# Kernel tuning notes

Hardware: AMD Instinct MI355X
Metric: run time of the kernel (lower is better)

The kernel has to match this reference:

```python
import jax, jax.numpy as jnp
import numpy as np

T, BATCH, DIM = 2048, 32, 512

def setup_inputs() -> dict:
    key = jax.random.key(0)
    ks = jax.random.split(key, 9)
    s = 1.0 / np.sqrt(DIM)
    return {
        "x": jax.random.normal(ks[0], (T, BATCH, DIM), dtype=jnp.float32),
        "W_in": jax.random.uniform(ks[1], (2 * DIM, DIM), jnp.float32, -s, s),
        "b_in": jax.random.uniform(ks[2], (2 * DIM,), jnp.float32, -s, s),
        "W_out": jax.random.uniform(ks[3], (DIM, DIM), jnp.float32, -s, s),
        "b_out": jax.random.uniform(ks[4], (DIM,), jnp.float32, -s, s),
        "A": jax.random.normal(ks[5], (DIM,), dtype=jnp.float32) * 0.1,
        "B": jax.random.normal(ks[6], (DIM,), dtype=jnp.float32) * 0.1,
        "gamma": jnp.ones((DIM,), dtype=jnp.float32),
        "beta": jnp.zeros((DIM,), dtype=jnp.float32),
    }

def _layernorm(y, gamma, beta, eps=1e-5):
    mu = jnp.mean(y, axis=-1, keepdims=True)
    var = jnp.mean(jnp.square(y - mu), axis=-1, keepdims=True)
    return (y - mu) * jax.lax.rsqrt(var + eps) * gamma + beta

def reference(x, W_in, b_in, W_out, b_out, A, B, gamma, beta):
    # in_proj then chunk along last dim: z first half, g second half
    zg = jnp.einsum('tbd,ed->tbe', x, W_in) + b_in          # [T,B,2D]
    z, g = jnp.split(zg, 2, axis=-1)
    g = jax.nn.sigmoid(g)
    Bz = B * z                                              # [T,B,D]
    gA = g * A                                              # [T,B,D]

    # diagonal linear recurrence h_t = gA_t * h_{t-1} + Bz_t
    def step(prev, inp):
        ga_t, bz_t = inp
        curr = ga_t * prev + bz_t
        return curr, curr

    h0 = jnp.zeros((x.shape[1], x.shape[2]), dtype=x.dtype)
    _, h = jax.lax.scan(step, h0, (gA, Bz))                 # [T,B,D]

    out = jnp.einsum('tbd,ed->tbe', h, W_out) + b_out
    return _layernorm(x + out, gamma, beta)
```

## Files before the change

kernel.cpp:

```cpp
#include <hip/hip_runtime.h>
#include <hip/hip_bf16.h>
#include <cstdint>
#include <cstddef>

#define T_LEN 2048
#define BATCH 32
#define DIM 512
#define M_TOT (T_LEN * BATCH)
#define K_DIM DIM
#define N1 (2 * DIM)
#define NCHUNK 64
#define CLEN (T_LEN / NCHUNK)
#define BD (BATCH * DIM)
#define MT256 (M_TOT / 256)

typedef unsigned short ushort_t;
typedef __attribute__((ext_vector_type(8))) short short8;
typedef __attribute__((ext_vector_type(4))) float floatx4;
typedef __attribute__((ext_vector_type(4))) unsigned short ushort4v;

__device__ __forceinline__ float bf2f(ushort_t u) {
  union { unsigned int i; float f; } v;
  v.i = ((unsigned int)u) << 16;
  return v.f;
}
__device__ __forceinline__ ushort_t f2bf(float f) {
  union { float f; unsigned int i; } v;
  v.f = f;
  unsigned int x = v.i;
  return (ushort_t)((x + 0x7fffu + ((x >> 16) & 1u)) >> 16);
}

__device__ __forceinline__ void async16(const void* gp, void* lp) {
  __builtin_amdgcn_global_load_lds(
      (__attribute__((address_space(1))) void*)(void*)gp,
      (__attribute__((address_space(3))) void*)lp, 16, 0, 0);
}

#define WAITVM(N) asm volatile("s_waitcnt vmcnt(" #N ")" ::: "memory")

__global__ __launch_bounds__(256) void cvt_f32_bf16(const float* __restrict__ in,
                                                    ushort_t* __restrict__ out,
                                                    int n4) {
  int i = blockIdx.x * 256 + threadIdx.x;
  if (i >= n4) return;
  const floatx4 v = *((const floatx4*)in + i);
  ushort4v o;
  o.x = f2bf(v.x); o.y = f2bf(v.y); o.z = f2bf(v.z); o.w = f2bf(v.w);
  *((ushort4v*)out + i) = o;
}

template <int MODE, int NT>
__global__ __launch_bounds__(512, 2) void gemm_bt(
    const ushort_t* __restrict__ Ag, const ushort_t* __restrict__ Bg,
    const float* __restrict__ bias, const float* __restrict__ Avec,
    const float* __restrict__ Bvec, ushort_t* __restrict__ out0,
    ushort_t* __restrict__ out1) {
  __shared__ __align__(16) ushort_t As[2][256 * 64];
  __shared__ __align__(16) ushort_t Bs[2][256 * 64];
  const int tid = threadIdx.x;
  const int lane = tid & 63;
  const int wid = tid >> 6;
  const int wave_m = wid >> 2;
  const int wave_n = wid & 3;

  const int bid = blockIdx.x;
  const int xcd = bid & 7;
  const int slot = bid >> 3;
  const int mt = xcd * (MT256 / 8) + slot / NT;
  const int nt = slot % NT;
  const int m0 = mt * 256;
  const int n0 = nt * 256;

  floatx4 acc[8][4] = {};

  const int sr = tid >> 3;
  const int sc = tid & 7;

  auto stage = [&](int kt, int s) {
    const int k0 = kt * 64;
#pragma unroll
    for (int i = 0; i < 4; i++) {
      const int r = i * 64 + sr;
      const int cg = sc ^ (r & 7);
      async16(Ag + (size_t)(m0 + r) * K_DIM + k0 + cg * 8,
              (char*)(&As[s][0]) + (i * 64 + wid * 8) * 128);
      async16(Bg + (size_t)(n0 + r) * K_DIM + k0 + cg * 8,
              (char*)(&Bs[s][0]) + (i * 64 + wid * 8) * 128);
    }
  };

  stage(0, 0);

  for (int t = 0; t < K_DIM / 64; ++t) {
    if (t < K_DIM / 64 - 1) {
      stage(t + 1, (t + 1) & 1);
      WAITVM(8);
    } else {
      WAITVM(0);
    }
    __builtin_amdgcn_s_barrier();
    __builtin_amdgcn_sched_barrier(0);

    const ushort_t* Asl = &As[t & 1][0];
    const ushort_t* Bsl = &Bs[t & 1][0];
#pragma unroll
    for (int kk = 0; kk < 2; kk++) {
      const int jc = kk * 4 + (lane >> 4);
      short8 af[8], bfr[4];
#pragma unroll
      for (int im = 0; im < 8; im++) {
        const int row = wave_m * 128 + im * 16 + (lane & 15);
        af[im] = *(const short8*)((const char*)Asl + row * 128 +
                                  ((jc ^ (row & 7)) * 16));
      }
#pragma unroll
      for (int in = 0; in < 4; in++) {
        const int row = wave_n * 64 + in * 16 + (lane & 15);
        bfr[in] = *(const short8*)((const char*)Bsl + row * 128 +
                                   ((jc ^ (row & 7)) * 16));
      }
#pragma unroll
      for (int im = 0; im < 8; im++)
#pragma unroll
        for (int in = 0; in < 4; in++)
          acc[im][in] = __builtin_amdgcn_mfma_f32_16x16x32_bf16(
              af[im], bfr[in], acc[im][in], 0, 0, 0);
    }
    __builtin_amdgcn_sched_barrier(0);
    __builtin_amdgcn_s_barrier();
  }

#pragma unroll
  for (int im = 0; im < 8; im++) {
#pragma unroll
    for (int in = 0; in < 4; in++) {
      const int col = n0 + wave_n * 64 + in * 16 + (lane & 15);
#pragma unroll
      for (int r = 0; r < 4; r++) {
        const int row = m0 + wave_m * 128 + im * 16 + (lane >> 4) * 4 + r;
        float val = acc[im][in][r] + bias[col];
        if (MODE == 0) {
          if (col < DIM) {
            out0[(size_t)row * DIM + col] = f2bf(Bvec[col] * val);
          } else {
            const int d = col - DIM;
            const float s = 1.f / (1.f + __expf(-val));
            out1[(size_t)row * DIM + d] = f2bf(Avec[d] * s);
          }
        } else {
          out0[(size_t)row * DIM + col] = f2bf(val);
        }
      }
    }
  }
}


__global__ __launch_bounds__(256) void scan_pass1(
    const ushort_t* __restrict__ a_arr, const ushort_t* __restrict__ bz_arr,
    float* __restrict__ pout, float* __restrict__ hout) {
  const int tid = blockIdx.x * 256 + threadIdx.x;
  const int c = tid >> 12;
  const int q = tid & 4095;
  size_t base = (size_t)(c * CLEN) * BD + q * 4;
  float h0 = 0.f, h1 = 0.f, h2 = 0.f, h3 = 0.f;
  float p0 = 1.f, p1 = 1.f, p2 = 1.f, p3 = 1.f;
#pragma unroll 8
  for (int t = 0; t < CLEN; t++) {
    ushort4v av = *(const ushort4v*)(a_arr + base + (size_t)t * BD);
    ushort4v bv = *(const ushort4v*)(bz_arr + base + (size_t)t * BD);
    float a0 = bf2f(av.x), a1 = bf2f(av.y), a2 = bf2f(av.z), a3 = bf2f(av.w);
    h0 = a0 * h0 + bf2f(bv.x); p0 *= a0;
    h1 = a1 * h1 + bf2f(bv.y); p1 *= a1;
    h2 = a2 * h2 + bf2f(bv.z); p2 *= a2;
    h3 = a3 * h3 + bf2f(bv.w); p3 *= a3;
  }
  const size_t ci = (size_t)c * BD + q * 4;
  *(floatx4*)(pout + ci) = (floatx4){p0, p1, p2, p3};
  *(floatx4*)(hout + ci) = (floatx4){h0, h1, h2, h3};
}

__global__ __launch_bounds__(256) void scan_pass2(
    const float* __restrict__ p, const float* __restrict__ hend,
    float* __restrict__ carry) {
  const int q = blockIdx.x * 256 + threadIdx.x;
  float h0 = 0.f, h1 = 0.f, h2 = 0.f, h3 = 0.f;
  for (int c = 0; c < NCHUNK; c++) {
    const size_t ci = (size_t)c * BD + q * 4;
    floatx4 pv = *(const floatx4*)(p + ci);
    floatx4 hv = *(const floatx4*)(hend + ci);
    *(floatx4*)(carry + ci) = (floatx4){h0, h1, h2, h3};
    h0 = hv.x + pv.x * h0;
    h1 = hv.y + pv.y * h1;
    h2 = hv.z + pv.z * h2;
    h3 = hv.w + pv.w * h3;
  }
}

__global__ __launch_bounds__(256) void scan_pass3(
    const ushort_t* __restrict__ a_arr, const ushort_t* __restrict__ bz_arr,
    const float* __restrict__ carry, ushort_t* __restrict__ h_arr) {
  const int tid = blockIdx.x * 256 + threadIdx.x;
  const int c = tid >> 12;
  const int q = tid & 4095;
  size_t base = (size_t)(c * CLEN) * BD + q * 4;
  const size_t ci = (size_t)c * BD + q * 4;
  floatx4 cv = *(const floatx4*)(carry + ci);
  float h0 = cv.x, h1 = cv.y, h2 = cv.z, h3 = cv.w;
#pragma unroll 8
  for (int t = 0; t < CLEN; t++) {
    ushort4v av = *(const ushort4v*)(a_arr + base + (size_t)t * BD);
    ushort4v bv = *(const ushort4v*)(bz_arr + base + (size_t)t * BD);
    h0 = bf2f(av.x) * h0 + bf2f(bv.x);
    h1 = bf2f(av.y) * h1 + bf2f(bv.y);
    h2 = bf2f(av.z) * h2 + bf2f(bv.z);
    h3 = bf2f(av.w) * h3 + bf2f(bv.w);
    ushort4v o;
    o.x = f2bf(h0); o.y = f2bf(h1); o.z = f2bf(h2); o.w = f2bf(h3);
    *(ushort4v*)(h_arr + base + (size_t)t * BD) = o;
  }
}

__global__ __launch_bounds__(256) void ln_kernel(
    const float* __restrict__ x, const ushort_t* __restrict__ op,
    const float* __restrict__ gamma, const float* __restrict__ beta,
    float* __restrict__ y) {
  const int wid = threadIdx.x >> 6;
  const int lane = threadIdx.x & 63;
  const size_t row = (size_t)blockIdx.x * 4 + wid;
  const size_t base = row * DIM + lane * 8;
  floatx4 x0 = *(const floatx4*)(x + base);
  floatx4 x1 = *(const floatx4*)(x + base + 4);
  short8 ov = *(const short8*)(op + base);
  float v[8];
  v[0] = x0.x + bf2f((ushort_t)ov[0]);
  v[1] = x0.y + bf2f((ushort_t)ov[1]);
  v[2] = x0.z + bf2f((ushort_t)ov[2]);
  v[3] = x0.w + bf2f((ushort_t)ov[3]);
  v[4] = x1.x + bf2f((ushort_t)ov[4]);
  v[5] = x1.y + bf2f((ushort_t)ov[5]);
  v[6] = x1.z + bf2f((ushort_t)ov[6]);
  v[7] = x1.w + bf2f((ushort_t)ov[7]);
  float s = 0.f, ss = 0.f;
#pragma unroll
  for (int j = 0; j < 8; j++) {
    s += v[j];
    ss += v[j] * v[j];
  }
#pragma unroll
  for (int m = 32; m >= 1; m >>= 1) {
    s += __shfl_xor(s, m, 64);
    ss += __shfl_xor(ss, m, 64);
  }
  const float mean = s * (1.f / DIM);
  const float var = ss * (1.f / DIM) - mean * mean;
  const float rstd = rsqrtf(var + 1e-5f);
  const int cb = lane * 8;
  floatx4 o0, o1;
  o0.x = (v[0] - mean) * rstd * gamma[cb + 0] + beta[cb + 0];
  o0.y = (v[1] - mean) * rstd * gamma[cb + 1] + beta[cb + 1];
  o0.z = (v[2] - mean) * rstd * gamma[cb + 2] + beta[cb + 2];
  o0.w = (v[3] - mean) * rstd * gamma[cb + 3] + beta[cb + 3];
  o1.x = (v[4] - mean) * rstd * gamma[cb + 4] + beta[cb + 4];
  o1.y = (v[5] - mean) * rstd * gamma[cb + 5] + beta[cb + 5];
  o1.z = (v[6] - mean) * rstd * gamma[cb + 6] + beta[cb + 6];
  o1.w = (v[7] - mean) * rstd * gamma[cb + 7] + beta[cb + 7];
  *(floatx4*)(y + base) = o0;
  *(floatx4*)(y + base + 4) = o1;
}

extern "C" void kernel_launch(void* const* d_in, const int* in_sizes, int n_in,
                              void* d_out, int out_size, void* d_ws,
                              size_t ws_size, hipStream_t stream) {
  const float* x = (const float*)d_in[0];
  const float* W_in = (const float*)d_in[1];
  const float* b_in = (const float*)d_in[2];
  const float* W_out = (const float*)d_in[3];
  const float* b_out = (const float*)d_in[4];
  const float* Avec = (const float*)d_in[5];
  const float* Bvec = (const float*)d_in[6];
  const float* gamma = (const float*)d_in[7];
  const float* beta = (const float*)d_in[8];
  float* out = (float*)d_out;

  char* ws = (char*)d_ws;
  const size_t SZ64 = (size_t)M_TOT * DIM * 2;
  ushort_t* xb = (ushort_t*)ws;
  ushort_t* gA = (ushort_t*)(ws + SZ64);
  ushort_t* bz = (ushort_t*)(ws + 2 * SZ64);
  ushort_t* wib = (ushort_t*)(ws + 3 * SZ64);
  ushort_t* wob = (ushort_t*)(ws + 3 * SZ64 + (size_t)N1 * K_DIM * 2);
  char* p0 = ws + 3 * SZ64 + (size_t)N1 * K_DIM * 2 + (size_t)DIM * K_DIM * 2;
  float* pc = (float*)p0;
  float* hc = (float*)(p0 + (size_t)NCHUNK * BD * 4);
  float* cc = (float*)(p0 + 2 * (size_t)NCHUNK * BD * 4);

  cvt_f32_bf16<<<(M_TOT * DIM / 4 + 255) / 256, 256, 0, stream>>>(
      x, xb, M_TOT * DIM / 4);
  cvt_f32_bf16<<<(N1 * K_DIM / 4 + 255) / 256, 256, 0, stream>>>(
      W_in, wib, N1 * K_DIM / 4);
  cvt_f32_bf16<<<(DIM * K_DIM / 4 + 255) / 256, 256, 0, stream>>>(
      W_out, wob, DIM * K_DIM / 4);

  gemm_bt<0, 4><<<MT256 * 4, 512, 0, stream>>>(
      xb, wib, b_in, Avec, Bvec, bz, gA);

  scan_pass1<<<NCHUNK * (BD / 4) / 256, 256, 0, stream>>>(gA, bz, pc, hc);
  scan_pass2<<<(BD / 4) / 256, 256, 0, stream>>>(pc, hc, cc);
  scan_pass3<<<NCHUNK * (BD / 4) / 256, 256, 0, stream>>>(gA, bz, cc, xb);

  gemm_bt<1, 2><<<MT256 * 2, 512, 0, stream>>>(
      xb, wob, b_out, nullptr, nullptr, gA, nullptr);

  ln_kernel<<<M_TOT / 4, 256, 0, stream>>>(x, gA, gamma, beta, out);
}
```

Baseline: 543.1 us.

## Split GEMM K-step into four phases interleaving LDS reads, prefetch and MFMA

Restructures the bf16 MFMA GEMM main loop into four phases per K tile. Each phase loads half the A fragments, issues part of the next tile's async global-to-LDS prefetch, then runs MFMAs at raised wave priority between barriers. This halves live A-fragment registers and spreads memory traffic across compute to improve overlap. The cost is more barriers per K step and a full vmcnt(0) wait before the next tile.

Measured after the change: 543.6 us. Within noise of the previous version (+0.1%).

```diff
diff --git a/kernel.cpp b/kernel.cpp
--- a/kernel.cpp
+++ b/kernel.cpp
@@ -37,7 +37,10 @@
       (__attribute__((address_space(3))) void*)lp, 16, 0, 0);
 }
 
-#define WAITVM(N) asm volatile("s_waitcnt vmcnt(" #N ")" ::: "memory")
+#define WAITVM0() asm volatile("s_waitcnt vmcnt(0)" ::: "memory")
+#define WAITLGKM0() asm volatile("s_waitcnt lgkmcnt(0)" ::: "memory")
+#define SBAR() __builtin_amdgcn_s_barrier()
+#define SCHED0() __builtin_amdgcn_sched_barrier(0)
 
 __global__ __launch_bounds__(256) void cvt_f32_bf16(const float* __restrict__ in,
                                                     ushort_t* __restrict__ out,
@@ -77,58 +80,68 @@
   const int sr = tid >> 3;
   const int sc = tid & 7;
 
-  auto stage = [&](int kt, int s) {
+  auto stage1 = [&](int kt, int s, int i) {
     const int k0 = kt * 64;
-#pragma unroll
-    for (int i = 0; i < 4; i++) {
-      const int r = i * 64 + sr;
-      const int cg = sc ^ (r & 7);
-      async16(Ag + (size_t)(m0 + r) * K_DIM + k0 + cg * 8,
-              (char*)(&As[s][0]) + (i * 64 + wid * 8) * 128);
-      async16(Bg + (size_t)(n0 + r) * K_DIM + k0 + cg * 8,
-              (char*)(&Bs[s][0]) + (i * 64 + wid * 8) * 128);
-    }
+    const int r = i * 64 + sr;
+    const int cg = sc ^ (r & 7);
+    async16(Ag + (size_t)(m0 + r) * K_DIM + k0 + cg * 8,
+            (char*)(&As[s][0]) + (i * 64 + wid * 8) * 128);
+    async16(Bg + (size_t)(n0 + r) * K_DIM + k0 + cg * 8,
+            (char*)(&Bs[s][0]) + (i * 64 + wid * 8) * 128);
   };
 
-  stage(0, 0);
+  stage1(0, 0, 0); stage1(0, 0, 1); stage1(0, 0, 2); stage1(0, 0, 3);
+  WAITVM0();
+  SBAR();
+
+  short8 bfr[4];
 
   for (int t = 0; t < K_DIM / 64; ++t) {
-    if (t < K_DIM / 64 - 1) {
-      stage(t + 1, (t + 1) & 1);
-      WAITVM(8);
-    } else {
-      WAITVM(0);
-    }
-    __builtin_amdgcn_s_barrier();
-    __builtin_amdgcn_sched_barrier(0);
-
-    const ushort_t* Asl = &As[t & 1][0];
-    const ushort_t* Bsl = &Bs[t & 1][0];
-#pragma unroll
-    for (int kk = 0; kk < 2; kk++) {
-      const int jc = kk * 4 + (lane >> 4);
-      short8 af[8], bfr[4];
-#pragma unroll
-      for (int im = 0; im < 8; im++) {
-        const int row = wave_m * 128 + im * 16 + (lane & 15);
-        af[im] = *(const short8*)((const char*)Asl + row * 128 +
-                                  ((jc ^ (row & 7)) * 16));
-      }
-#pragma unroll
-      for (int in = 0; in < 4; in++) {
-        const int row = wave_n * 64 + in * 16 + (lane & 15);
-        bfr[in] = *(const short8*)((const char*)Bsl + row * 128 +
-                                   ((jc ^ (row & 7)) * 16));
-      }
-#pragma unroll
-      for (int im = 0; im < 8; im++)
-#pragma unroll
-        for (int in = 0; in < 4; in++)
-          acc[im][in] = __builtin_amdgcn_mfma_f32_16x16x32_bf16(
-              af[im], bfr[in], acc[im][in], 0, 0, 0);
-    }
-    __builtin_amdgcn_sched_barrier(0);
-    __builtin_amdgcn_s_barrier();
+    const int p = t & 1;
+    const ushort_t* Asl = &As[p][0];
+    const ushort_t* Bsl = &Bs[p][0];
+    const bool pre = (t < K_DIM / 64 - 1);
+
+#define PHASE(KK, IMB, LDB, DO_STAGE, SI0, SI1, LASTSYNC)                     \
+  {                                                                           \
+    const int jc = (KK)*4 + (lane >> 4);                                      \
+    short8 af[4];                                                             \
+    if (LDB) {                                                                \
+      _Pragma("unroll") for (int in = 0; in < 4; in++) {                      \
+        const int row = wave_n * 64 + in * 16 + (lane & 15);                  \
+        bfr[in] = *(const short8*)((const char*)Bsl + row * 128 +             \
+                                   ((jc ^ (row & 7)) * 16));                  \
+      }                                                                       \
+    }                                                                         \
+    _Pragma("unroll") for (int q = 0; q < 4; q++) {                           \
+      const int row = wave_m * 128 + ((IMB) + q) * 16 + (lane & 15);          \
+      af[q] = *(const short8*)((const char*)Asl + row * 128 +                 \
+                               ((jc ^ (row & 7)) * 16));                      \
+    }                                                                         \
+    if ((DO_STAGE) && pre) {                                                  \
+      stage1(t + 1, p ^ 1, SI0);                                              \
+      stage1(t + 1, p ^ 1, SI1);                                              \
+    }                                                                         \
+    SCHED0();                                                                 \
+    SBAR();                                                                   \
+    WAITLGKM0();                                                              \
+    SCHED0();                                                                 \
+    __builtin_amdgcn_s_setprio(1);                                            \
+    _Pragma("unroll") for (int q = 0; q < 4; q++)                             \
+        _Pragma("unroll") for (int in = 0; in < 4; in++)                      \
+            acc[(IMB) + q][in] = __builtin_amdgcn_mfma_f32_16x16x32_bf16(     \
+                af[q], bfr[in], acc[(IMB) + q][in], 0, 0, 0);                 \
+    __builtin_amdgcn_s_setprio(0);                                            \
+    SCHED0();                                                                 \
+    if ((LASTSYNC) && pre) WAITVM0();                                         \
+    SBAR();                                                                   \
+  }
+
+    PHASE(0, 0, true,  true,  0, 1, false)
+    PHASE(0, 4, false, true,  2, 3, false)
+    PHASE(1, 0, true,  false, 0, 0, false)
+    PHASE(1, 4, false, false, 0, 0, true)
+#undef PHASE
   }
 
 #pragma unroll
```
